# Optimization experiments

Measured on AMD Instinct MI355X. Metric: run time of the kernel, lower is better.

## Reference

```python
import jax, jax.numpy as jnp
import numpy as np

DIM = 256
HEADS = 8
HEAD_DIM = DIM // HEADS
HIDDEN = DIM * 4


def layer_norm(x, w, b, eps=1e-5):
    m = jnp.mean(x, axis=-1, keepdims=True)
    v = jnp.mean((x - m) ** 2, axis=-1, keepdims=True)
    return (x - m) / jnp.sqrt(v + eps) * w + b


def setup_inputs() -> dict:
    key = jax.random.key(0)
    ks = jax.random.split(key, 12)
    s = lambda fan_in: 1.0 / np.sqrt(fan_in)
    inp = {
        "x0": jax.random.normal(ks[0], (2, 32, 64, DIM), jnp.float32),
        "x1": jax.random.normal(ks[1], (2, 32, 64, DIM), jnp.float32),
        # torch Linear weights stored [out, in], no bias for qk/v/merge
        "qk_w": jax.random.uniform(ks[2], (DIM, DIM), jnp.float32, -s(DIM), s(DIM)),
        "v_w": jax.random.uniform(ks[3], (DIM, DIM), jnp.float32, -s(DIM), s(DIM)),
        "merge_w": jax.random.uniform(ks[4], (DIM, DIM), jnp.float32, -s(DIM), s(DIM)),
        "ln1_w": jnp.ones((DIM,), jnp.float32),
        "ln1_b": jnp.zeros((DIM,), jnp.float32),
        "ln2_w": jnp.ones((DIM,), jnp.float32),
        "ln2_b": jnp.zeros((DIM,), jnp.float32),
        "fc1_w": jax.random.uniform(ks[5], (HIDDEN, 2 * DIM), jnp.float32, -s(2 * DIM), s(2 * DIM)),
        "fc1_b": jnp.zeros((HIDDEN,), jnp.float32),
        "fc2_w": jax.random.uniform(ks[6], (DIM, HIDDEN), jnp.float32, -s(HIDDEN), s(HIDDEN)),
        "fc2_b": jnp.zeros((DIM,), jnp.float32),
        "gamma": jnp.ones((DIM,), jnp.float32),
    }
    return inp


def reference(x0, x1, qk_w, v_w, merge_w, ln1_w, ln1_b, ln2_w, ln2_b,
              fc1_w, fc1_b, fc2_w, fc2_b, gamma):
    N0, L0, WW0, C = x0.shape
    N1, L1, WW1, _ = x1.shape
    x0f = x0.reshape(N0, L0 * WW0, C)
    x1f = x1.reshape(N1, L1 * WW1, C)

    n0 = layer_norm(x0f, ln1_w, ln1_b)
    n1 = layer_norm(x1f, ln1_w, ln1_b)

    def heads(t):  # [N, S, C] -> [N, H, S, Dh]
        N, S, _ = t.shape
        return t.reshape(N, S, HEADS, HEAD_DIM).transpose(0, 2, 1, 3)

    scale = HEAD_DIM ** -0.25  # sqrt of softmax_temp, applied to both sides
    qk0 = heads(n0 @ qk_w.T) * scale
    qk1 = heads(n1 @ qk_w.T) * scale
    v0 = heads(n0 @ v_w.T)
    v1 = heads(n1 @ v_w.T)

    # shared score matrix, reused for both softmax directions
    sim = jnp.einsum('bhld,bhsd->bhls', qk0, qk1)  # [N,H,L,S]
    attn01 = jax.nn.softmax(sim, axis=-1)
    attn10 = jax.nn.softmax(sim, axis=-2)  # == softmax(sim^T, -1)^T

    m0 = jnp.einsum('bhls,bhsd->bhld', attn01, v1)
    m1 = jnp.einsum('bhls,bhld->bhsd', attn10, v0)

    def unheads(t):  # [N,H,S,Dh] -> [N,S,C]
        N, H, S, D = t.shape
        return t.transpose(0, 2, 1, 3).reshape(N, S, H * D)

    m0 = unheads(m0) @ merge_w.T
    m1 = unheads(m1) @ merge_w.T

    def ffn_residual(x, m):
        h = jnp.concatenate([x, m], axis=-1)
        h = jax.nn.gelu(h @ fc1_w.T + fc1_b, approximate=False)
        h = h @ fc2_w.T + fc2_b
        return x + gamma * layer_norm(h, ln2_w, ln2_b)

    y0 = ffn_residual(x0f, m0).reshape(N0, L0, WW0, C)
    y1 = ffn_residual(x1f, m1).reshape(N1, L1, WW1, C)
    return (y0, y1)
```

## Files before the change

kernel.cpp:

```cpp
#include <hip/hip_runtime.h>
#include <hip/hip_bf16.h>
#include <math.h>


typedef float  f32x4  __attribute__((ext_vector_type(4)));
typedef __bf16 bf16x8 __attribute__((ext_vector_type(8)));

#define MFMA16(A, B, C) __builtin_amdgcn_mfma_f32_16x16x32_bf16((A), (B), (C), 0, 0, 0)

static constexpr int   ROWS  = 8192;
static constexpr float QK_SCALE = 0.42044820762685725f;

__device__ inline unsigned short f2b(float f) {
    __hip_bfloat16 h = __float2bfloat16(f);
    union { __hip_bfloat16 h; unsigned short u; } cv;
    cv.h = h;
    return cv.u;
}

__device__ inline float gelu_f(float x) {
    float z = 0.7978845608028654f * (x + 0.044715f * x * x * x);
    z = fminf(fmaxf(z, -15.0f), 15.0f);
    const float e = __expf(-2.0f * z);
    const float t = (1.0f - e) / (1.0f + e);
    return 0.5f * x * (1.0f + t);
}

__global__ __launch_bounds__(256) void cvt_w_kernel(
    const float* __restrict__ qkw, const float* __restrict__ vw,
    const float* __restrict__ mw,  const float* __restrict__ w1,
    const float* __restrict__ w2,  unsigned short* __restrict__ o)
{
    int i = blockIdx.x * 256 + threadIdx.x;
    float v;
    if      (i <  65536) v = qkw[i];
    else if (i < 131072) v = vw[i - 65536];
    else if (i < 196608) v = mw[i - 131072];
    else if (i < 720896) v = w1[i - 196608];
    else                 v = w2[i - 720896];
    o[i] = f2b(v);
}

__global__ __launch_bounds__(256) void ln_in_kernel(
    const float* __restrict__ x0, const float* __restrict__ x1,
    const float* __restrict__ w,  const float* __restrict__ b,
    unsigned short* __restrict__ nb,
    unsigned short* __restrict__ acat)
{
    const int wid  = threadIdx.x >> 6;
    const int lane = threadIdx.x & 63;
    const int row  = blockIdx.x * 4 + wid;
    const float* xr = (row < 4096) ? (x0 + (size_t)row * 256)
                                   : (x1 + (size_t)(row - 4096) * 256);
    const int c0 = lane * 4;
    const float4 xv = *(const float4*)(xr + c0);
    float s  = (xv.x + xv.y) + (xv.z + xv.w);
    float sq = (xv.x * xv.x + xv.y * xv.y) + (xv.z * xv.z + xv.w * xv.w);
#pragma unroll
    for (int off = 1; off < 64; off <<= 1) {
        s  += __shfl_xor(s,  off);
        sq += __shfl_xor(sq, off);
    }
    const float mean = s * (1.0f / 256.0f);
    const float var  = sq * (1.0f / 256.0f) - mean * mean;
    const float rs   = rsqrtf(var + 1e-5f);
    const float4 wv4 = *(const float4*)(w + c0);
    const float4 bv4 = *(const float4*)(b + c0);
    ushort4 nv;
    nv.x = f2b((xv.x - mean) * rs * wv4.x + bv4.x);
    nv.y = f2b((xv.y - mean) * rs * wv4.y + bv4.y);
    nv.z = f2b((xv.z - mean) * rs * wv4.z + bv4.z);
    nv.w = f2b((xv.w - mean) * rs * wv4.w + bv4.w);
    *(ushort4*)(nb + (size_t)row * 256 + c0) = nv;
    ushort4 xb;
    xb.x = f2b(xv.x); xb.y = f2b(xv.y); xb.z = f2b(xv.z); xb.w = f2b(xv.w);
    *(ushort4*)(acat + (size_t)row * 512 + c0) = xb;
}

__global__ __launch_bounds__(256) void gemm_qkv(
    const unsigned short* __restrict__ A, const unsigned short* __restrict__ W,
    unsigned short* __restrict__ qkb, unsigned short* __restrict__ vtb)
{
    constexpr int K = 256;
    __shared__ unsigned short As[64 * 72];
    __shared__ unsigned short Ws[64 * 72];
    const int tid  = threadIdx.x;
    const int wid  = tid >> 6;
    const int lane = tid & 63;
    const int ln   = lane & 15;
    const int quad = lane >> 4;
    const int m0 = blockIdx.x * 64, n0 = blockIdx.y * 64;
    f32x4 acc[4] = {{0,0,0,0},{0,0,0,0},{0,0,0,0},{0,0,0,0}};
    const int srow = tid >> 3;
    const int skc  = (tid & 7) * 8;
    const unsigned short* aP0 = A + (size_t)(m0 + srow)      * K + skc;
    const unsigned short* aP1 = A + (size_t)(m0 + srow + 32) * K + skc;
    const unsigned short* wP0 = W + (size_t)(n0 + srow)      * K + skc;
    const unsigned short* wP1 = W + (size_t)(n0 + srow + 32) * K + skc;
    for (int k0 = 0; k0 < K; k0 += 64) {
        *(uint4*)(As + srow * 72 + skc)        = *(const uint4*)(aP0 + k0);
        *(uint4*)(As + (srow + 32) * 72 + skc) = *(const uint4*)(aP1 + k0);
        *(uint4*)(Ws + srow * 72 + skc)        = *(const uint4*)(wP0 + k0);
        *(uint4*)(Ws + (srow + 32) * 72 + skc) = *(const uint4*)(wP1 + k0);
        __syncthreads();
#pragma unroll
        for (int kk = 0; kk < 64; kk += 32) {
            const bf16x8 af = *(const bf16x8*)(As + (wid * 16 + ln) * 72 + kk + quad * 8);
#pragma unroll
            for (int f = 0; f < 4; ++f) {
                const bf16x8 wf = *(const bf16x8*)(Ws + (f * 16 + ln) * 72 + kk + quad * 8);
                acc[f] = MFMA16(wf, af, acc[f]);
            }
        }
        __syncthreads();
    }
    const int rowm = m0 + wid * 16 + ln;
    if (n0 < 256) {
#pragma unroll
        for (int f = 0; f < 4; ++f) {
            const int cb = n0 + f * 16 + quad * 4;
            ushort4 o;
            o.x = f2b(acc[f][0] * QK_SCALE); o.y = f2b(acc[f][1] * QK_SCALE);
            o.z = f2b(acc[f][2] * QK_SCALE); o.w = f2b(acc[f][3] * QK_SCALE);
            *(ushort4*)(qkb + (size_t)rowm * 256 + cb) = o;
        }
    } else {
#pragma unroll
        for (int f = 0; f < 4; ++f) {
            const int cb = (n0 - 256) + f * 16 + quad * 4;
#pragma unroll
            for (int r = 0; r < 4; ++r)
                vtb[(size_t)(cb + r) * 8192 + rowm] = f2b(acc[f][r]);
        }
    }
}

__global__ __launch_bounds__(256) void gemm_merge(
    const unsigned short* __restrict__ A, const unsigned short* __restrict__ W,
    unsigned short* __restrict__ outB)
{
    constexpr int K = 256;
    __shared__ unsigned short As[64 * 72];
    __shared__ unsigned short Ws[64 * 72];
    const int tid  = threadIdx.x;
    const int wid  = tid >> 6;
    const int lane = tid & 63;
    const int ln   = lane & 15;
    const int quad = lane >> 4;
    const int m0 = blockIdx.x * 64, n0 = blockIdx.y * 64;
    f32x4 acc[4] = {{0,0,0,0},{0,0,0,0},{0,0,0,0},{0,0,0,0}};
    const int srow = tid >> 3;
    const int skc  = (tid & 7) * 8;
    const unsigned short* aP0 = A + (size_t)(m0 + srow)      * K + skc;
    const unsigned short* aP1 = A + (size_t)(m0 + srow + 32) * K + skc;
    const unsigned short* wP0 = W + (size_t)(n0 + srow)      * K + skc;
    const unsigned short* wP1 = W + (size_t)(n0 + srow + 32) * K + skc;
    for (int k0 = 0; k0 < K; k0 += 64) {
        *(uint4*)(As + srow * 72 + skc)        = *(const uint4*)(aP0 + k0);
        *(uint4*)(As + (srow + 32) * 72 + skc) = *(const uint4*)(aP1 + k0);
        *(uint4*)(Ws + srow * 72 + skc)        = *(const uint4*)(wP0 + k0);
        *(uint4*)(Ws + (srow + 32) * 72 + skc) = *(const uint4*)(wP1 + k0);
        __syncthreads();
#pragma unroll
        for (int kk = 0; kk < 64; kk += 32) {
            const bf16x8 af = *(const bf16x8*)(As + (wid * 16 + ln) * 72 + kk + quad * 8);
#pragma unroll
            for (int f = 0; f < 4; ++f) {
                const bf16x8 wf = *(const bf16x8*)(Ws + (f * 16 + ln) * 72 + kk + quad * 8);
                acc[f] = MFMA16(wf, af, acc[f]);
            }
        }
        __syncthreads();
    }
    const int rowm = m0 + wid * 16 + ln;
#pragma unroll
    for (int f = 0; f < 4; ++f) {
        const int cb = n0 + f * 16 + quad * 4;
        ushort4 o;
        o.x = f2b(acc[f][0]); o.y = f2b(acc[f][1]);
        o.z = f2b(acc[f][2]); o.w = f2b(acc[f][3]);
        *(ushort4*)(outB + (size_t)rowm * 512 + 256 + cb) = o;
    }
}

template <bool GELU_, bool OUTB>
__global__ __launch_bounds__(256) void gemm128(
    const unsigned short* __restrict__ A, const unsigned short* __restrict__ W,
    const float* __restrict__ bias,
    unsigned short* __restrict__ outB, float* __restrict__ outF,
    int K, int NS)
{
    __shared__ unsigned short As[128 * 72];
    __shared__ unsigned short Ws[128 * 72];
    const int tid  = threadIdx.x;
    const int wid  = tid >> 6;
    const int lane = tid & 63;
    const int ln   = lane & 15;
    const int quad = lane >> 4;
    const int m0 = blockIdx.x * 128, n0 = blockIdx.y * 128;
    const int wm = (wid & 1) * 64, wn = (wid >> 1) * 64;
    f32x4 acc[4][4];
#pragma unroll
    for (int f = 0; f < 4; ++f)
#pragma unroll
        for (int i = 0; i < 4; ++i) acc[f][i] = (f32x4){0, 0, 0, 0};
    const int sr = tid >> 2;
    const int sc = (tid & 3) * 8;
    for (int k0 = 0; k0 < K; k0 += 64) {
        const unsigned short* aB = A + (size_t)m0 * K + k0;
        const unsigned short* wB = W + (size_t)n0 * K + k0;
        *(uint4*)(As + sr * 72 + sc)             = *(const uint4*)(aB + (size_t)sr * K + sc);
        *(uint4*)(As + sr * 72 + sc + 32)        = *(const uint4*)(aB + (size_t)sr * K + sc + 32);
        *(uint4*)(As + (sr + 64) * 72 + sc)      = *(const uint4*)(aB + (size_t)(sr + 64) * K + sc);
        *(uint4*)(As + (sr + 64) * 72 + sc + 32) = *(const uint4*)(aB + (size_t)(sr + 64) * K + sc + 32);
        *(uint4*)(Ws + sr * 72 + sc)             = *(const uint4*)(wB + (size_t)sr * K + sc);
        *(uint4*)(Ws + sr * 72 + sc + 32)        = *(const uint4*)(wB + (size_t)sr * K + sc + 32);
        *(uint4*)(Ws + (sr + 64) * 72 + sc)      = *(const uint4*)(wB + (size_t)(sr + 64) * K + sc);
        *(uint4*)(Ws + (sr + 64) * 72 + sc + 32) = *(const uint4*)(wB + (size_t)(sr + 64) * K + sc + 32);
        __syncthreads();
#pragma unroll
        for (int kk = 0; kk < 64; kk += 32) {
            bf16x8 af[4], wf[4];
#pragma unroll
            for (int i = 0; i < 4; ++i)
                af[i] = *(const bf16x8*)(As + (wm + i * 16 + ln) * 72 + kk + quad * 8);
#pragma unroll
            for (int f = 0; f < 4; ++f)
                wf[f] = *(const bf16x8*)(Ws + (wn + f * 16 + ln) * 72 + kk + quad * 8);
#pragma unroll
            for (int f = 0; f < 4; ++f)
#pragma unroll
                for (int i = 0; i < 4; ++i)
                    acc[f][i] = MFMA16(wf[f], af[i], acc[f][i]);
        }
        __syncthreads();
    }
#pragma unroll
    for (int f = 0; f < 4; ++f) {
        const int feat = n0 + wn + f * 16 + quad * 4;
        const float4 b4 = *(const float4*)(bias + feat);
#pragma unroll
        for (int i = 0; i < 4; ++i) {
            const int token = m0 + wm + i * 16 + ln;
            float vv[4] = {acc[f][i][0] + b4.x, acc[f][i][1] + b4.y,
                           acc[f][i][2] + b4.z, acc[f][i][3] + b4.w};
            if (GELU_) {
#pragma unroll
                for (int r = 0; r < 4; ++r) vv[r] = gelu_f(vv[r]);
            }
            if (OUTB) {
                ushort4 o;
                o.x = f2b(vv[0]); o.y = f2b(vv[1]); o.z = f2b(vv[2]); o.w = f2b(vv[3]);
                *(ushort4*)(outB + (size_t)token * NS + feat) = o;
            } else {
                float4 o = {vv[0], vv[1], vv[2], vv[3]};
                *(float4*)(outF + (size_t)token * NS + feat) = o;
            }
        }
    }
}

__global__ __launch_bounds__(256) void attn_kernel(
    const unsigned short* __restrict__ qk, const unsigned short* __restrict__ vtb,
    unsigned short* __restrict__ mo)
{
    __shared__ unsigned short Kl[128 * 40];
    __shared__ unsigned short Vt[32 * 136];
    __shared__ unsigned short Pl[4][16 * 136];
    const int tid  = threadIdx.x;
    const int wid  = tid >> 6;
    const int lane = tid & 63;
    const int ln   = lane & 15;
    const int quad = lane >> 4;
    const int dir = blockIdx.z, bh = blockIdx.y;
    const int b = bh >> 3, h = bh & 7;
    const int qbase = b * 2048 + (dir ? 4096 : 0);
    const int kbase = b * 2048 + (dir ? 0 : 4096);
    const int q0 = blockIdx.x * 64;

    const bf16x8 qf =
        *(const bf16x8*)(qk + (size_t)(qbase + q0 + wid * 16 + ln) * 256 + h * 32 + quad * 8);

    f32x4 oacc[2] = {{0,0,0,0},{0,0,0,0}};
    float lpart = 0.0f;
    const f32x4 zf = {0,0,0,0};
    const int krow = tid >> 2;
    const int kc8  = (tid & 3) * 8;
    const int vd   = tid >> 3;
    const int vk8  = (tid & 7) * 8;
    const unsigned short* vRow = vtb + (size_t)(h * 32 + vd) * 8192;

    for (int kt = 0; kt < 16; ++kt) {
        const int kpos = kbase + kt * 128;
        *(uint4*)(Kl + krow * 40 + kc8) =
            *(const uint4*)(qk + (size_t)(kpos + krow) * 256 + h * 32 + kc8);
        *(uint4*)(Kl + (krow + 64) * 40 + kc8) =
            *(const uint4*)(qk + (size_t)(kpos + krow + 64) * 256 + h * 32 + kc8);
        *(uint4*)(Vt + vd * 136 + vk8)      = *(const uint4*)(vRow + kpos + vk8);
        *(uint4*)(Vt + vd * 136 + vk8 + 64) = *(const uint4*)(vRow + kpos + vk8 + 64);
        __syncthreads();

#pragma unroll
        for (int sub = 0; sub < 8; ++sub) {
            const bf16x8 kf = *(const bf16x8*)(Kl + (sub * 16 + ln) * 40 + quad * 8);
            f32x4 s = MFMA16(kf, qf, zf);
            const float e0 = __expf(s[0]), e1 = __expf(s[1]);
            const float e2 = __expf(s[2]), e3 = __expf(s[3]);
            lpart += (e0 + e1) + (e2 + e3);
            ushort4 pb;
            pb.x = f2b(e0); pb.y = f2b(e1); pb.z = f2b(e2); pb.w = f2b(e3);
            *(ushort4*)(&Pl[wid][ln * 136 + sub * 16 + quad * 4]) = pb;
        }
        asm volatile("s_waitcnt lgkmcnt(0)" ::: "memory");

#pragma unroll
        for (int koff = 0; koff < 128; koff += 32) {
            const bf16x8 pf = *(const bf16x8*)(&Pl[wid][ln * 136 + koff + quad * 8]);
#pragma unroll
            for (int dg = 0; dg < 2; ++dg) {
                const bf16x8 vf = *(const bf16x8*)(Vt + (dg * 16 + ln) * 136 + koff + quad * 8);
                oacc[dg] = MFMA16(vf, pf, oacc[dg]);
            }
        }
        __syncthreads();
    }

    lpart += __shfl_xor(lpart, 16);
    lpart += __shfl_xor(lpart, 32);
    const float rinv = 1.0f / lpart;

    const size_t orow = (size_t)(qbase + q0 + wid * 16 + ln) * 256 + h * 32;
#pragma unroll
    for (int dg = 0; dg < 2; ++dg) {
        ushort4 o;
        o.x = f2b(oacc[dg][0] * rinv);
        o.y = f2b(oacc[dg][1] * rinv);
        o.z = f2b(oacc[dg][2] * rinv);
        o.w = f2b(oacc[dg][3] * rinv);
        *(ushort4*)(mo + orow + dg * 16 + quad * 4) = o;
    }
}

__global__ __launch_bounds__(256) void ln_out_kernel(
    const float* __restrict__ x0, const float* __restrict__ x1,
    const float* __restrict__ h2, const float* __restrict__ w,
    const float* __restrict__ b,  const float* __restrict__ gamma,
    float* __restrict__ out)
{
    const int wid  = threadIdx.x >> 6;
    const int lane = threadIdx.x & 63;
    const int row  = blockIdx.x * 4 + wid;
    const int c0 = lane * 4;
    const float4 hv = *(const float4*)(h2 + (size_t)row * 256 + c0);
    float s  = (hv.x + hv.y) + (hv.z + hv.w);
    float sq = (hv.x * hv.x + hv.y * hv.y) + (hv.z * hv.z + hv.w * hv.w);
#pragma unroll
    for (int off = 1; off < 64; off <<= 1) {
        s  += __shfl_xor(s,  off);
        sq += __shfl_xor(sq, off);
    }
    const float mean = s * (1.0f / 256.0f);
    const float var  = sq * (1.0f / 256.0f) - mean * mean;
    const float rs   = rsqrtf(var + 1e-5f);
    const float* xr = (row < 4096) ? (x0 + (size_t)row * 256)
                                   : (x1 + (size_t)(row - 4096) * 256);
    const float4 xv = *(const float4*)(xr + c0);
    const float4 w4 = *(const float4*)(w + c0);
    const float4 b4 = *(const float4*)(b + c0);
    const float4 g4 = *(const float4*)(gamma + c0);
    float4 y;
    y.x = xv.x + g4.x * ((hv.x - mean) * rs * w4.x + b4.x);
    y.y = xv.y + g4.y * ((hv.y - mean) * rs * w4.y + b4.y);
    y.z = xv.z + g4.z * ((hv.z - mean) * rs * w4.z + b4.z);
    y.w = xv.w + g4.w * ((hv.w - mean) * rs * w4.w + b4.w);
    *(float4*)(out + (size_t)row * 256 + c0) = y;
}

extern "C" void kernel_launch(void* const* d_in, const int* in_sizes, int n_in,
                              void* d_out, int out_size, void* d_ws, size_t ws_size,
                              hipStream_t stream) {
    (void)in_sizes; (void)n_in; (void)out_size; (void)ws_size;
    const float* x0      = (const float*)d_in[0];
    const float* x1      = (const float*)d_in[1];
    const float* qk_w    = (const float*)d_in[2];
    const float* v_w     = (const float*)d_in[3];
    const float* merge_w = (const float*)d_in[4];
    const float* ln1_w   = (const float*)d_in[5];
    const float* ln1_b   = (const float*)d_in[6];
    const float* ln2_w   = (const float*)d_in[7];
    const float* ln2_b   = (const float*)d_in[8];
    const float* fc1_w   = (const float*)d_in[9];
    const float* fc1_b   = (const float*)d_in[10];
    const float* fc2_w   = (const float*)d_in[11];
    const float* fc2_b   = (const float*)d_in[12];
    const float* gamma   = (const float*)d_in[13];
    float* out = (float*)d_out;

    unsigned short* nb   = (unsigned short*)d_ws;
    unsigned short* qkb  = nb   + (size_t)ROWS * 256;
    unsigned short* vtb  = qkb  + (size_t)ROWS * 256;
    unsigned short* mb   = vtb  + (size_t)ROWS * 256;
    unsigned short* acat = mb   + (size_t)ROWS * 256;
    unsigned short* fc1o = acat + (size_t)ROWS * 512;
    float*          h2   = (float*)(fc1o + (size_t)ROWS * 1024);
    unsigned short* wqv  = (unsigned short*)(h2 + (size_t)ROWS * 256);
    unsigned short* wm   = wqv + 131072;
    unsigned short* w1   = wm  + 65536;
    unsigned short* w2   = w1  + 524288;

    cvt_w_kernel<<<3840, 256, 0, stream>>>(qk_w, v_w, merge_w, fc1_w, fc2_w, wqv);
    ln_in_kernel<<<2048, 256, 0, stream>>>(x0, x1, ln1_w, ln1_b, nb, acat);

    gemm_qkv<<<dim3(128, 8), 256, 0, stream>>>(nb, wqv, qkb, vtb);

    attn_kernel<<<dim3(32, 16, 2), 256, 0, stream>>>(qkb, vtb, mb);

    gemm_merge<<<dim3(128, 4), 256, 0, stream>>>(mb, wm, acat);

    gemm128<true, true><<<dim3(64, 8), 256, 0, stream>>>(
        acat, w1, fc1_b, fc1o, nullptr, 512, 1024);
    gemm128<false, false><<<dim3(64, 2), 256, 0, stream>>>(
        fc1o, w2, fc2_b, nullptr, h2, 1024, 256);

    ln_out_kernel<<<2048, 256, 0, stream>>>(x0, x1, h2, ln2_w, ln2_b, gamma, out);
}
```

Measured before the change: 191.2 us.

## Split attention keys across waves with register-direct K/V and cross-wave reduction

The attention kernel changes how work is split across waves: each wave now covers all 64 queries of the block and owns a quarter of the key range. K and V fragments load straight from global memory into registers with one-step prefetch, so the shared-memory K/V tiles and the per-tile block barriers go away. Partial outputs and row sums are combined through shared memory at the end. The exp is swapped for a raw v_exp_f32 exp2 with log2(e) folded into the QK scale, and launch bounds ask for 4 blocks per SM; in exchange there are more registers per thread and an extra reduction phase with several barriers.

```diff
diff --git a/kernel.cpp b/kernel.cpp
--- a/kernel.cpp
+++ b/kernel.cpp
@@ -9,13 +9,19 @@
 #define MFMA16(A, B, C) __builtin_amdgcn_mfma_f32_16x16x32_bf16((A), (B), (C), 0, 0, 0)
 
 static constexpr int   ROWS  = 8192;
-static constexpr float QK_SCALE = 0.42044820762685725f;
+static constexpr float QK_SCALE = 0.42044820762685725f * 1.2011224087864498f;
 
 __device__ inline unsigned short f2b(float f) {
     __hip_bfloat16 h = __float2bfloat16(f);
     union { __hip_bfloat16 h; unsigned short u; } cv;
     cv.h = h;
     return cv.u;
+}
+
+__device__ inline float exp2_fast(float x) {
+    float r;
+    asm("v_exp_f32 %0, %1\n\ts_nop 0" : "=v"(r) : "v"(x));
+    return r;
 }
 
 __device__ inline float gelu_f(float x) {
@@ -260,13 +266,11 @@
     }
 }
 
-__global__ __launch_bounds__(256) void attn_kernel(
+__global__ __launch_bounds__(256, 4) void attn_kernel(
     const unsigned short* __restrict__ qk, const unsigned short* __restrict__ vtb,
     unsigned short* __restrict__ mo)
 {
-    __shared__ unsigned short Kl[128 * 40];
-    __shared__ unsigned short Vt[32 * 136];
-    __shared__ unsigned short Pl[4][16 * 136];
+    __shared__ unsigned short Pw[4][64 * 40];
     const int tid  = threadIdx.x;
     const int wid  = tid >> 6;
     const int lane = tid & 63;
@@ -277,67 +281,107 @@
     const int qbase = b * 2048 + (dir ? 4096 : 0);
     const int kbase = b * 2048 + (dir ? 0 : 4096);
     const int q0 = blockIdx.x * 64;
-
-    const bf16x8 qf =
-        *(const bf16x8*)(qk + (size_t)(qbase + q0 + wid * 16 + ln) * 256 + h * 32 + quad * 8);
-
-    f32x4 oacc[2] = {{0,0,0,0},{0,0,0,0}};
-    float lpart = 0.0f;
-    const f32x4 zf = {0,0,0,0};
-    const int krow = tid >> 2;
-    const int kc8  = (tid & 3) * 8;
-    const int vd   = tid >> 3;
-    const int vk8  = (tid & 7) * 8;
-    const unsigned short* vRow = vtb + (size_t)(h * 32 + vd) * 8192;
-
-    for (int kt = 0; kt < 16; ++kt) {
-        const int kpos = kbase + kt * 128;
-        *(uint4*)(Kl + krow * 40 + kc8) =
-            *(const uint4*)(qk + (size_t)(kpos + krow) * 256 + h * 32 + kc8);
-        *(uint4*)(Kl + (krow + 64) * 40 + kc8) =
-            *(const uint4*)(qk + (size_t)(kpos + krow + 64) * 256 + h * 32 + kc8);
-        *(uint4*)(Vt + vd * 136 + vk8)      = *(const uint4*)(vRow + kpos + vk8);
-        *(uint4*)(Vt + vd * 136 + vk8 + 64) = *(const uint4*)(vRow + kpos + vk8 + 64);
-        __syncthreads();
-
-#pragma unroll
-        for (int sub = 0; sub < 8; ++sub) {
-            const bf16x8 kf = *(const bf16x8*)(Kl + (sub * 16 + ln) * 40 + quad * 8);
-            f32x4 s = MFMA16(kf, qf, zf);
-            const float e0 = __expf(s[0]), e1 = __expf(s[1]);
-            const float e2 = __expf(s[2]), e3 = __expf(s[3]);
-            lpart += (e0 + e1) + (e2 + e3);
-            ushort4 pb;
-            pb.x = f2b(e0); pb.y = f2b(e1); pb.z = f2b(e2); pb.w = f2b(e3);
-            *(ushort4*)(&Pl[wid][ln * 136 + sub * 16 + quad * 4]) = pb;
+    const int xsw = (ln & 3) << 3;
+
+    bf16x8 qf[4];
+#pragma unroll
+    for (int qg = 0; qg < 4; ++qg)
+        qf[qg] = *(const bf16x8*)(qk + (size_t)(qbase + q0 + qg * 16 + ln) * 256 + h * 32 + quad * 8);
+
+    f32x4 oacc[4][2];
+#pragma unroll
+    for (int qg = 0; qg < 4; ++qg) {
+        oacc[qg][0] = (f32x4){0, 0, 0, 0};
+        oacc[qg][1] = (f32x4){0, 0, 0, 0};
+    }
+    float lp[4] = {0.0f, 0.0f, 0.0f, 0.0f};
+    const f32x4 zf = {0, 0, 0, 0};
+
+    const unsigned short* kp = qk  + (size_t)(kbase + wid * 32 + ln) * 256 + h * 32 + quad * 8;
+    const unsigned short* vp = vtb + (size_t)(h * 32 + ln) * 8192 + (kbase + wid * 32) + quad * 8;
+
+    unsigned short* Pq[4];
+#pragma unroll
+    for (int qg = 0; qg < 4; ++qg) Pq[qg] = &Pw[wid][(qg * 16 + ln) * 40];
+
+    bf16x8 kc0 = *(const bf16x8*)(kp);
+    bf16x8 kc1 = *(const bf16x8*)(kp + 16 * 256);
+    bf16x8 vc0 = *(const bf16x8*)(vp);
+    bf16x8 vc1 = *(const bf16x8*)(vp + 16 * 8192);
+    bf16x8 vn0, vn1;
+
+    for (int it = 0; it < 16; ++it) {
+#pragma unroll
+        for (int sub = 0; sub < 2; ++sub) {
+            const bf16x8 kf = sub ? kc1 : kc0;
+            f32x4 s[4];
+#pragma unroll
+            for (int qg = 0; qg < 4; ++qg) s[qg] = MFMA16(kf, qf[qg], zf);
+#pragma unroll
+            for (int qg = 0; qg < 4; ++qg) {
+                const float e0 = exp2_fast(s[qg][0]), e1 = exp2_fast(s[qg][1]);
+                const float e2 = exp2_fast(s[qg][2]), e3 = exp2_fast(s[qg][3]);
+                lp[qg] += (e0 + e1) + (e2 + e3);
+                ushort4 pb;
+                pb.x = f2b(e0); pb.y = f2b(e1); pb.z = f2b(e2); pb.w = f2b(e3);
+                *(ushort4*)(Pq[qg] + ((sub * 16 + quad * 4) ^ xsw)) = pb;
+            }
+        }
+        if (it < 15) {
+            const unsigned short* kn = kp + (size_t)(it + 1) * 128 * 256;
+            const unsigned short* vn = vp + (it + 1) * 128;
+            kc0 = *(const bf16x8*)(kn);
+            kc1 = *(const bf16x8*)(kn + 16 * 256);
+            vn0 = *(const bf16x8*)(vn);
+            vn1 = *(const bf16x8*)(vn + 16 * 8192);
         }
         asm volatile("s_waitcnt lgkmcnt(0)" ::: "memory");
-
-#pragma unroll
-        for (int koff = 0; koff < 128; koff += 32) {
-            const bf16x8 pf = *(const bf16x8*)(&Pl[wid][ln * 136 + koff + quad * 8]);
+#pragma unroll
+        for (int qg = 0; qg < 4; ++qg) {
+            const bf16x8 pf = *(const bf16x8*)(Pq[qg] + ((quad * 8) ^ xsw));
+            oacc[qg][0] = MFMA16(vc0, pf, oacc[qg][0]);
+            oacc[qg][1] = MFMA16(vc1, pf, oacc[qg][1]);
+        }
+        if (it < 15) { vc0 = vn0; vc1 = vn1; }
+    }
+
+#pragma unroll
+    for (int qg = 0; qg < 4; ++qg) {
+        lp[qg] += __shfl_xor(lp[qg], 16);
+        lp[qg] += __shfl_xor(lp[qg], 32);
+    }
+    __syncthreads();
+    float* scr  = (float*)&Pw[0][0];
+    float* Lbuf = scr;
+    float* Obuf = scr + 256;
+    if (quad == 0) {
+#pragma unroll
+        for (int qg = 0; qg < 4; ++qg) Lbuf[wid * 64 + qg * 16 + ln] = lp[qg];
+    }
+#pragma unroll
+    for (int qg = 0; qg < 4; ++qg) {
+#pragma unroll
+        for (int dg = 0; dg < 2; ++dg)
+            *(f32x4*)&Obuf[(wid * 2 + dg) * 256 + lane * 4] = oacc[qg][dg];
+        __syncthreads();
+        if (wid == qg) {
+            const int q = qg * 16 + ln;
+            const float rinv = 1.0f /
+                (Lbuf[q] + Lbuf[64 + q] + Lbuf[128 + q] + Lbuf[192 + q]);
+            const size_t orow = (size_t)(qbase + q0 + q) * 256 + h * 32;
 #pragma unroll
             for (int dg = 0; dg < 2; ++dg) {
-                const bf16x8 vf = *(const bf16x8*)(Vt + (dg * 16 + ln) * 136 + koff + quad * 8);
-                oacc[dg] = MFMA16(vf, pf, oacc[dg]);
-            }
-        }
-        __syncthreads();
-    }
-
-    lpart += __shfl_xor(lpart, 16);
-    lpart += __shfl_xor(lpart, 32);
-    const float rinv = 1.0f / lpart;
-
-    const size_t orow = (size_t)(qbase + q0 + wid * 16 + ln) * 256 + h * 32;
-#pragma unroll
-    for (int dg = 0; dg < 2; ++dg) {
-        ushort4 o;
-        o.x = f2b(oacc[dg][0] * rinv);
-        o.y = f2b(oacc[dg][1] * rinv);
-        o.z = f2b(oacc[dg][2] * rinv);
-        o.w = f2b(oacc[dg][3] * rinv);
-        *(ushort4*)(mo + orow + dg * 16 + quad * 4) = o;
+                f32x4 sum = *(f32x4*)&Obuf[(0 + dg) * 256 + lane * 4];
+#pragma unroll
+                for (int w = 1; w < 4; ++w)
+                    sum += *(f32x4*)&Obuf[(w * 2 + dg) * 256 + lane * 4];
+                ushort4 o;
+                o.x = f2b(sum[0] * rinv); o.y = f2b(sum[1] * rinv);
+                o.z = f2b(sum[2] * rinv); o.w = f2b(sum[3] * rinv);
+                *(ushort4*)(mo + orow + dg * 16 + quad * 4) = o;
+            }
+        }
+        __syncthreads();
     }
 }
 
```

New measurement: 186.5 us. -2.4%, faster.
